# Kernel optimization log

Measured on AMD Instinct MI355X. Metric: run time of the kernel, lower is better.

The kernel has to match this reference:

```python
import jax, jax.numpy as jnp
import numpy as np

N_NODES = 512
IN_FEATURES = 512
N_HEADS = 8
N_HIDDEN = 64  # out_features // n_heads
NEG_SLOPE = 0.2


def setup_inputs() -> dict:
    key = jax.random.key(0)
    k_h, k_ws, k_wt, k_a, k_adj = jax.random.split(key, 5)
    lim_w = 1.0 / np.sqrt(IN_FEATURES)
    lim_a = 1.0 / np.sqrt(N_HIDDEN)
    h = jax.random.normal(k_h, (1, N_NODES, IN_FEATURES), dtype=jnp.float32)
    # nn.Linear weights: [out, in]
    W_source = jax.random.uniform(k_ws, (N_HEADS * N_HIDDEN, IN_FEATURES), jnp.float32, -lim_w, lim_w)
    W_target = jax.random.uniform(k_wt, (N_HEADS * N_HIDDEN, IN_FEATURES), jnp.float32, -lim_w, lim_w)
    attn_w = jax.random.uniform(k_a, (N_HIDDEN,), jnp.float32, -lim_a, lim_a)  # Linear(n_hidden, 1)
    adjacency_matrix = jax.random.randint(k_adj, (N_NODES, N_NODES, 1), 0, 2, dtype=jnp.int32)
    return {"h": h, "W_source": W_source, "W_target": W_target,
            "attn_w": attn_w, "adjacency_matrix": adjacency_matrix}


def reference(h, W_source, W_target, attn_w, adjacency_matrix):
    n_nodes = h.shape[1]
    x = h[0]  # [N, D]; module assumes batch == 1
    g_source = (x @ W_source.T).reshape(n_nodes, N_HEADS, N_HIDDEN)  # [N,H,F]
    g_target = (x @ W_target.T).reshape(n_nodes, N_HEADS, N_HIDDEN)  # [N,H,F]
    # g_sum[i, j] = g_source[j] + g_target[i]  (repeat / repeat_interleave semantics)
    g_sum = g_source[None, :, :, :] + g_target[:, None, :, :]  # [N,N,H,F]
    act = jnp.where(g_sum >= 0, g_sum, NEG_SLOPE * g_sum)       # LeakyReLU
    scores = jnp.einsum('ijhf,f->ijh', act, attn_w)              # [N,N,H]
    scores = jnp.where(adjacency_matrix == 0, -jnp.inf, scores)  # adj broadcasts over heads
    attention = jax.nn.softmax(scores, axis=1)                   # softmax over source nodes j
    # dropout p applied at eval -> identity
    head_output = jnp.einsum('ijh,jhf->ihf', attention, g_target)  # [N,H,F]
    out = head_output.reshape(n_nodes, N_HEADS * N_HIDDEN)         # is_concat=True
    return out, attention
```

## Files before the change

### kernel.cpp

```cpp
#include <hip/hip_runtime.h>

#define NN 512
#define IND 512
#define NH 8
#define NF 64

__global__ __launch_bounds__(256) void gemm_nt(
    const float* __restrict__ Aa, const float* __restrict__ Ba, float* __restrict__ Ca,
    const float* __restrict__ Ab, const float* __restrict__ Bb, float* __restrict__ Cb)
{
    const float* A = blockIdx.z ? Ab : Aa;
    const float* B = blockIdx.z ? Bb : Ba;
    float*       C = blockIdx.z ? Cb : Ca;

    __shared__ __align__(16) float Vs[2][32][132];
    __shared__ float2 sp[2][4][64];

    const int tid  = threadIdx.x;
    const int wv   = __builtin_amdgcn_readfirstlane(tid >> 6);
    const int lane = tid & 63;
    const int rg = wv & 1, kh = wv >> 1;
    const int r0 = blockIdx.y * 8 + rg * 4;
    const int c0 = blockIdx.x * 128;

    const float* Sp = A + (size_t)r0 * IND + kh * 256;
    const int ts = tid & 127;
    const float* Brow = B + (size_t)(c0 + ts) * IND + kh * 256;

    float2 a0 = {0.f,0.f}, a1 = {0.f,0.f}, a2 = {0.f,0.f}, a3 = {0.f,0.f};

    for (int ch = 0; ch < 8; ++ch) {
        float4 f[8];
        const float4* bp = reinterpret_cast<const float4*>(Brow + ch * 32);
        #pragma unroll
        for (int i = 0; i < 8; ++i) f[i] = bp[i];
        __syncthreads();
        #pragma unroll
        for (int i = 0; i < 8; ++i) {
            Vs[kh][i * 4 + 0][ts] = f[i].x;
            Vs[kh][i * 4 + 1][ts] = f[i].y;
            Vs[kh][i * 4 + 2][ts] = f[i].z;
            Vs[kh][i * 4 + 3][ts] = f[i].w;
        }
        __syncthreads();
        const float* Spc = Sp + ch * 32;
        #pragma unroll 8
        for (int kk = 0; kk < 32; ++kk) {
            float2 v = *reinterpret_cast<const float2*>(&Vs[kh][kk][lane * 2]);
            float s0 = Spc[kk];
            float s1 = Spc[IND + kk];
            float s2 = Spc[2 * IND + kk];
            float s3 = Spc[3 * IND + kk];
            a0.x = fmaf(s0, v.x, a0.x); a0.y = fmaf(s0, v.y, a0.y);
            a1.x = fmaf(s1, v.x, a1.x); a1.y = fmaf(s1, v.y, a1.y);
            a2.x = fmaf(s2, v.x, a2.x); a2.y = fmaf(s2, v.y, a2.y);
            a3.x = fmaf(s3, v.x, a3.x); a3.y = fmaf(s3, v.y, a3.y);
        }
    }

    if (kh) {
        sp[rg][0][lane] = a0; sp[rg][1][lane] = a1;
        sp[rg][2][lane] = a2; sp[rg][3][lane] = a3;
    }
    __syncthreads();
    if (!kh) {
        float2 p;
        const int cc = c0 + lane * 2;
        p = sp[rg][0][lane]; a0.x += p.x; a0.y += p.y;
        p = sp[rg][1][lane]; a1.x += p.x; a1.y += p.y;
        p = sp[rg][2][lane]; a2.x += p.x; a2.y += p.y;
        p = sp[rg][3][lane]; a3.x += p.x; a3.y += p.y;
        *reinterpret_cast<float2*>(C + (size_t)(r0 + 0) * NN + cc) = a0;
        *reinterpret_cast<float2*>(C + (size_t)(r0 + 1) * NN + cc) = a1;
        *reinterpret_cast<float2*>(C + (size_t)(r0 + 2) * NN + cc) = a2;
        *reinterpret_cast<float2*>(C + (size_t)(r0 + 3) * NN + cc) = a3;
    }
}

__global__ __launch_bounds__(512) void gat_attn(
    const float* __restrict__ Gs_t,
    const float* __restrict__ Gt,
    const float* __restrict__ attn_w,
    const int*   __restrict__ adj,
    float* __restrict__ out_feat,
    float* __restrict__ out_att)
{
    __shared__ float s_sc[8][512];
    __shared__ float s_red[8][8][64];

    const int tid = threadIdx.x;
    const int i0  = blockIdx.x * 8;
    const int h   = blockIdx.y;

    {
        const int j = tid;
        float acc[8];
        #pragma unroll
        for (int i = 0; i < 8; ++i) acc[i] = 0.f;
        float p = 0.f;
        const float* gsp = Gs_t + (size_t)h * NF * NN + j;
        const float* gtp = Gt + (size_t)i0 * IND + h * NF;
        #pragma unroll 4
        for (int f = 0; f < NF; ++f) {
            float w = attn_w[f];
            float g = gsp[(size_t)f * NN];
            p = fmaf(w, g, p);
            #pragma unroll
            for (int i = 0; i < 8; ++i) {
                float t = g + gtp[(size_t)i * IND + f];
                acc[i] = fmaf(w, fabsf(t), acc[i]);
            }
        }
        const float px = 0.6f * p;
        #pragma unroll
        for (int i = 0; i < 8; ++i) {
            int ad = adj[(size_t)(i0 + i) * NN + j];
            s_sc[i][j] = ad ? fmaf(0.4f, acc[i], px) : -INFINITY;
        }
    }
    __syncthreads();

    {
        const int w = tid >> 6, lane = tid & 63;
        float m = -INFINITY;
        #pragma unroll
        for (int r = 0; r < 8; ++r) m = fmaxf(m, s_sc[w][lane + r * 64]);
        #pragma unroll
        for (int off = 32; off >= 1; off >>= 1) m = fmaxf(m, __shfl_xor(m, off, 64));
        float e[8];
        float sum = 0.f;
        #pragma unroll
        for (int r = 0; r < 8; ++r) {
            float ev = __expf(s_sc[w][lane + r * 64] - m);
            e[r] = ev;
            sum += ev;
        }
        #pragma unroll
        for (int off = 32; off >= 1; off >>= 1) sum += __shfl_xor(sum, off, 64);
        float inv = 1.f / sum;
        const int i = i0 + w;
        #pragma unroll
        for (int r = 0; r < 8; ++r) {
            int j = lane + r * 64;
            float a = e[r] * inv;
            s_sc[w][j] = a;
            out_att[((size_t)i * NN + j) * NH + h] = a;
        }
    }
    __syncthreads();

    {
        const int w = tid >> 6, lane = tid & 63;
        const int jb = w * 64;
        float o[8];
        #pragma unroll
        for (int i = 0; i < 8; ++i) o[i] = 0.f;
        const float* gtc = Gt + h * NF + lane;
        #pragma unroll 2
        for (int s = 0; s < 16; ++s) {
            const int j = jb + 4 * s;
            float4 b[8];
            #pragma unroll
            for (int i = 0; i < 8; ++i)
                b[i] = *reinterpret_cast<const float4*>(&s_sc[i][j]);
            float gv;
            gv = gtc[(size_t)(j + 0) * IND];
            #pragma unroll
            for (int i = 0; i < 8; ++i) o[i] = fmaf(b[i].x, gv, o[i]);
            gv = gtc[(size_t)(j + 1) * IND];
            #pragma unroll
            for (int i = 0; i < 8; ++i) o[i] = fmaf(b[i].y, gv, o[i]);
            gv = gtc[(size_t)(j + 2) * IND];
            #pragma unroll
            for (int i = 0; i < 8; ++i) o[i] = fmaf(b[i].z, gv, o[i]);
            gv = gtc[(size_t)(j + 3) * IND];
            #pragma unroll
            for (int i = 0; i < 8; ++i) o[i] = fmaf(b[i].w, gv, o[i]);
        }
        #pragma unroll
        for (int i = 0; i < 8; ++i) s_red[w][i][lane] = o[i];
    }
    __syncthreads();
    {
        const int ii = tid >> 6, f = tid & 63;
        float s = 0.f;
        #pragma unroll
        for (int w = 0; w < 8; ++w) s += s_red[w][ii][f];
        out_feat[(size_t)(i0 + ii) * (NH * NF) + h * NF + f] = s;
    }
}

extern "C" void kernel_launch(void* const* d_in, const int* in_sizes, int n_in,
                              void* d_out, int out_size, void* d_ws, size_t ws_size,
                              hipStream_t stream) {
    const float* X   = (const float*)d_in[0];
    const float* Ws  = (const float*)d_in[1];
    const float* Wtg = (const float*)d_in[2];
    const float* aw  = (const float*)d_in[3];
    const int*   adj = (const int*)d_in[4];

    float* Gs_t = (float*)d_ws;
    float* Gt   = Gs_t + (size_t)NN * IND;

    float* out_feat = (float*)d_out;
    float* out_att  = out_feat + (size_t)NN * NH * NF;

    hipLaunchKernelGGL(gemm_nt, dim3(4, 64, 2), dim3(256), 0, stream,
                       Ws, X, Gs_t, X, Wtg, Gt);
    hipLaunchKernelGGL(gat_attn, dim3(NN / 8, NH), dim3(512), 0, stream,
                       Gs_t, Gt, aw, adj, out_feat, out_att);
}
```

Baseline: 107.2 us.

## Double-buffer GEMM shared tile with register prefetch and larger blocks

```diff
diff --git a/kernel.cpp b/kernel.cpp
--- a/kernel.cpp
+++ b/kernel.cpp
@@ -5,7 +5,7 @@
 #define NH 8
 #define NF 64
 
-__global__ __launch_bounds__(256) void gemm_nt(
+__global__ __launch_bounds__(512) void gemm_nt(
     const float* __restrict__ Aa, const float* __restrict__ Ba, float* __restrict__ Ca,
     const float* __restrict__ Ab, const float* __restrict__ Bb, float* __restrict__ Cb)
 {
@@ -13,40 +13,51 @@
     const float* B = blockIdx.z ? Bb : Ba;
     float*       C = blockIdx.z ? Cb : Ca;
 
-    __shared__ __align__(16) float Vs[2][32][132];
-    __shared__ float2 sp[2][4][64];
+    __shared__ __align__(16) float Vs[2][2][32][132];
+    __shared__ float2 sp[4][4][64];
 
     const int tid  = threadIdx.x;
     const int wv   = __builtin_amdgcn_readfirstlane(tid >> 6);
     const int lane = tid & 63;
-    const int rg = wv & 1, kh = wv >> 1;
-    const int r0 = blockIdx.y * 8 + rg * 4;
+    const int rg = wv & 3, kh = wv >> 2;
+    const int r0 = blockIdx.y * 16 + rg * 4;
     const int c0 = blockIdx.x * 128;
 
     const float* Sp = A + (size_t)r0 * IND + kh * 256;
-    const int ts = tid & 127;
-    const float* Brow = B + (size_t)(c0 + ts) * IND + kh * 256;
+
+    const int ts = tid & 255;
+    const int sc = ts & 127;
+    const int kq = ts >> 7;
+    const float* Brow = B + (size_t)(c0 + sc) * IND + kh * 256 + kq * 16;
 
     float2 a0 = {0.f,0.f}, a1 = {0.f,0.f}, a2 = {0.f,0.f}, a3 = {0.f,0.f};
 
+    float4 f[4];
+    {
+        const float4* bp = reinterpret_cast<const float4*>(Brow);
+        #pragma unroll
+        for (int i = 0; i < 4; ++i) f[i] = bp[i];
+        #pragma unroll
+        for (int i = 0; i < 4; ++i) {
+            Vs[0][kh][kq * 16 + i * 4 + 0][sc] = f[i].x;
+            Vs[0][kh][kq * 16 + i * 4 + 1][sc] = f[i].y;
+            Vs[0][kh][kq * 16 + i * 4 + 2][sc] = f[i].z;
+            Vs[0][kh][kq * 16 + i * 4 + 3][sc] = f[i].w;
+        }
+    }
+
     for (int ch = 0; ch < 8; ++ch) {
-        float4 f[8];
-        const float4* bp = reinterpret_cast<const float4*>(Brow + ch * 32);
-        #pragma unroll
-        for (int i = 0; i < 8; ++i) f[i] = bp[i];
-        __syncthreads();
-        #pragma unroll
-        for (int i = 0; i < 8; ++i) {
-            Vs[kh][i * 4 + 0][ts] = f[i].x;
-            Vs[kh][i * 4 + 1][ts] = f[i].y;
-            Vs[kh][i * 4 + 2][ts] = f[i].z;
-            Vs[kh][i * 4 + 3][ts] = f[i].w;
+        if (ch < 7) {
+            const float4* bp = reinterpret_cast<const float4*>(Brow + (ch + 1) * 32);
+            #pragma unroll
+            for (int i = 0; i < 4; ++i) f[i] = bp[i];
         }
         __syncthreads();
         const float* Spc = Sp + ch * 32;
+        const float (*V)[132] = Vs[ch & 1][kh];
         #pragma unroll 8
         for (int kk = 0; kk < 32; ++kk) {
-            float2 v = *reinterpret_cast<const float2*>(&Vs[kh][kk][lane * 2]);
+            float2 v = *reinterpret_cast<const float2*>(&V[kk][lane * 2]);
             float s0 = Spc[kk];
             float s1 = Spc[IND + kk];
             float s2 = Spc[2 * IND + kk];
@@ -55,6 +66,15 @@
             a1.x = fmaf(s1, v.x, a1.x); a1.y = fmaf(s1, v.y, a1.y);
             a2.x = fmaf(s2, v.x, a2.x); a2.y = fmaf(s2, v.y, a2.y);
             a3.x = fmaf(s3, v.x, a3.x); a3.y = fmaf(s3, v.y, a3.y);
+        }
+        if (ch < 7) {
+            #pragma unroll
+            for (int i = 0; i < 4; ++i) {
+                Vs[(ch + 1) & 1][kh][kq * 16 + i * 4 + 0][sc] = f[i].x;
+                Vs[(ch + 1) & 1][kh][kq * 16 + i * 4 + 1][sc] = f[i].y;
+                Vs[(ch + 1) & 1][kh][kq * 16 + i * 4 + 2][sc] = f[i].z;
+                Vs[(ch + 1) & 1][kh][kq * 16 + i * 4 + 3][sc] = f[i].w;
+            }
         }
     }
 
@@ -205,7 +225,7 @@
     float* out_feat = (float*)d_out;
     float* out_att  = out_feat + (size_t)NN * NH * NF;
 
-    hipLaunchKernelGGL(gemm_nt, dim3(4, 64, 2), dim3(256), 0, stream,
+    hipLaunchKernelGGL(gemm_nt, dim3(4, 32, 2), dim3(512), 0, stream,
                        Ws, X, Gs_t, X, Wtg, Gt);
     hipLaunchKernelGGL(gat_attn, dim3(NN / 8, NH), dim3(512), 0, stream,
                        Gs_t, Gt, aw, adj, out_feat, out_att);
```

New measurement: 103.3 us, median of 2. 1.04x faster.
